# Kernel optimization log

Measured on AMD Instinct MI355X. Metric: run time of the kernel, lower is better.

## Reference

```python
import jax, jax.numpy as jnp
import numpy as np

B, S, D, H = 2, 2048, 1024, 16
HD = D // H  # head dim = 64

def setup_inputs() -> dict:
    key = jax.random.key(0)
    ks = jax.random.split(key, 3)
    scale = 1.0 / np.sqrt(D)
    return {
        "x": jax.random.normal(ks[0], (B, S, D), jnp.float32),
        "W_attn": jax.random.normal(ks[1], (D, 3 * D), jnp.float32) * scale,
        "b_attn": jnp.zeros((3 * D,), jnp.float32),
        "W_proj": jax.random.normal(ks[2], (D, D), jnp.float32) * scale,
        "b_proj": jnp.zeros((D,), jnp.float32),
    }

def reference(x, W_attn, b_attn, W_proj, b_proj):
    b, s, d = x.shape
    qkv = x @ W_attn + b_attn                      # [B,S,3D]
    q, k, v = jnp.split(qkv, 3, axis=-1)
    # [B,S,D] -> [B,H,S,HD]
    def heads(t):
        return t.reshape(b, s, H, HD).transpose(0, 2, 1, 3)
    q, k, v = heads(q), heads(k), heads(v)
    scores = jnp.einsum('bhqd,bhkd->bhqk', q, k) * (1.0 / np.sqrt(HD))
    causal = jnp.tril(jnp.ones((s, s), dtype=bool))
    scores = jnp.where(causal[None, None], scores, -jnp.inf)
    probs = jax.nn.softmax(scores, axis=-1)
    y = jnp.einsum('bhqk,bhkd->bhqd', probs, v)    # [B,H,S,HD]
    y = y.transpose(0, 2, 1, 3).reshape(b, s, d)
    return y @ W_proj + b_proj
```

## Files before the change

kernel.cpp:

```cpp
#include <hip/hip_runtime.h>

typedef __bf16 bf16;
typedef __bf16 bf16x4 __attribute__((ext_vector_type(4)));
typedef __bf16 bf16x8 __attribute__((ext_vector_type(8)));
typedef float f32x4 __attribute__((ext_vector_type(4)));

#define S_LEN 2048
#define D_DIM 1024
#define N_HEAD 16
#define HEAD_DIM 64
#define M_TOK 4096
#define BH 32

#define EXP2F(x) __builtin_amdgcn_exp2f(x)
#define Q_SCALE 0.18033688f

typedef __attribute__((address_space(3))) void lds_void;
typedef const __attribute__((address_space(1))) void gbl_void;

__device__ __forceinline__ void gl_lds16(const bf16* g, bf16* l) {
  __builtin_amdgcn_global_load_lds((gbl_void*)g, (lds_void*)l, 16, 0, 0);
}

__global__ __launch_bounds__(256) void k_cast(const float* __restrict__ x,
                                              bf16* __restrict__ o, int n) {
  int i = (blockIdx.x * 256 + threadIdx.x) * 4;
  if (i >= n) return;
  float4 v = *(const float4*)(x + i);
  bf16x4 w;
  w[0] = (bf16)v.x; w[1] = (bf16)v.y; w[2] = (bf16)v.z; w[3] = (bf16)v.w;
  *(bf16x4*)(o + i) = w;
}

__global__ __launch_bounds__(256) void k_transpose(const float* __restrict__ W,
                                                   bf16* __restrict__ Wt,
                                                   int K, int N) {
  __shared__ float tile[32][33];
  int nb = blockIdx.x, kb = blockIdx.y;
  int t = threadIdx.x;
  int r = t >> 3, c4 = (t & 7) * 4;
  float4 v = *(const float4*)&W[(kb * 32 + r) * N + nb * 32 + c4];
  tile[r][c4 + 0] = v.x; tile[r][c4 + 1] = v.y;
  tile[r][c4 + 2] = v.z; tile[r][c4 + 3] = v.w;
  __syncthreads();
  bf16x4 o;
  #pragma unroll
  for (int i = 0; i < 4; i++) o[i] = (bf16)tile[c4 + i][r];
  *(bf16x4*)&Wt[(nb * 32 + r) * K + kb * 32 + c4] = o;
}

__global__ __launch_bounds__(256, 2)
void k_gemm_qkv(const bf16* __restrict__ A, const bf16* __restrict__ Bt,
                const float* __restrict__ bias,
                bf16* __restrict__ qk, bf16* __restrict__ vT) {
  __shared__ bf16 As[128 * 32];
  __shared__ bf16 Bs[128 * 32];
  const int K = 1024;
  int bn = blockIdx.x, bm = blockIdx.y;
  int t = threadIdx.x;
  int wave = t >> 6, lane = t & 63, c = lane & 15, quad = lane >> 4;
  int wm = wave & 1, wn = wave >> 1;
  int ldrow = lane >> 2, ldcol = (lane & 3) * 8;

  const bf16* Ag = A + (size_t)(bm * 128) * K;
  const bf16* Bg = Bt + (size_t)(bn * 128) * K;

  f32x4 acc[4][4] = {};

  for (int k0 = 0; k0 < K; k0 += 32) {
    __syncthreads();
    #pragma unroll
    for (int q = 0; q < 2; q++) {
      int r0 = (wave * 2 + q) * 16;
      gl_lds16(&Ag[(size_t)(r0 + ldrow) * K + k0 + ldcol], &As[r0 * 32]);
      gl_lds16(&Bg[(size_t)(r0 + ldrow) * K + k0 + ldcol], &Bs[r0 * 32]);
    }
    __syncthreads();
    bf16x8 af[4];
    #pragma unroll
    for (int mt = 0; mt < 4; mt++)
      af[mt] = *(const bf16x8*)&As[(wm * 64 + mt * 16 + c) * 32 + quad * 8];
    #pragma unroll
    for (int nt = 0; nt < 4; nt++) {
      bf16x8 bfr = *(const bf16x8*)&Bs[(wn * 64 + nt * 16 + c) * 32 + quad * 8];
      #pragma unroll
      for (int mt = 0; mt < 4; mt++)
        acc[mt][nt] = __builtin_amdgcn_mfma_f32_16x16x32_bf16(af[mt], bfr, acc[mt][nt], 0, 0, 0);
    }
  }

  #pragma unroll
  for (int nt = 0; nt < 4; nt++) {
    int n = bn * 128 + wn * 64 + nt * 16 + c;
    int which = n >> 10, nl = n & 1023;
    int h = nl >> 6, hd = nl & 63;
    float bv = bias[n];
    #pragma unroll
    for (int mt = 0; mt < 4; mt++) {
      int m0 = bm * 128 + wm * 64 + mt * 16 + quad * 4;
      int b = m0 >> 11, s0 = m0 & 2047;
      int bh = b * N_HEAD + h;
      if (which == 2) {
        bf16x4 o;
        #pragma unroll
        for (int r = 0; r < 4; r++) o[r] = (bf16)(acc[mt][nt][r] + bv);
        *(bf16x4*)&vT[((size_t)bh * HEAD_DIM + hd) * S_LEN + s0] = o;
      } else if (which == 0) {
        #pragma unroll
        for (int r = 0; r < 4; r++)
          qk[(bh * S_LEN + s0 + r) * HEAD_DIM + hd] = (bf16)((acc[mt][nt][r] + bv) * Q_SCALE);
      } else {
        #pragma unroll
        for (int r = 0; r < 4; r++)
          qk[BH * S_LEN * HEAD_DIM + (bh * S_LEN + s0 + r) * HEAD_DIM + hd] = (bf16)(acc[mt][nt][r] + bv);
      }
    }
  }
}

__global__ __launch_bounds__(256, 2)
void k_attn(const bf16* __restrict__ qk, const bf16* __restrict__ vT,
            bf16* __restrict__ y) {
  __shared__ bf16 Ks[64][72];
  __shared__ bf16 Vs[64][72];
  __shared__ bf16 Ps[128][72];
  int bx = blockIdx.x;
  int bh = bx & 31;
  int tile = 15 - (bx >> 5);
  int t = threadIdx.x, w = t >> 6, lane = t & 63, c = lane & 15, quad = lane >> 4;
  const bf16* Qg = qk + (size_t)bh * (S_LEN * HEAD_DIM);
  const bf16* Kg = qk + (size_t)(BH + bh) * (S_LEN * HEAD_DIM);
  const bf16* Vg = vT + (size_t)bh * (HEAD_DIM * S_LEN);
  int b = bh >> 4, h = bh & 15;
  int srow = t >> 3, scol = (t & 7) * 8;

  int qA = tile * 128 + w * 16;
  int qB = qA + 64;
  int nkb = 2 * tile + 2;
  int dthr = w * 16 + c;

  bf16x8 qfA0 = *(const bf16x8*)&Qg[(qA + c) * HEAD_DIM + quad * 8];
  bf16x8 qfA1 = *(const bf16x8*)&Qg[(qA + c) * HEAD_DIM + 32 + quad * 8];
  bf16x8 qfB0 = *(const bf16x8*)&Qg[(qB + c) * HEAD_DIM + quad * 8];
  bf16x8 qfB1 = *(const bf16x8*)&Qg[(qB + c) * HEAD_DIM + 32 + quad * 8];

  float mA = -1e30f, lA = 0.f, mB = -1e30f, lB = 0.f;
  f32x4 accA[4] = {}, accB[4] = {};

  bf16x8 kr0 = *(const bf16x8*)&Kg[srow * HEAD_DIM + scol];
  bf16x8 kr1 = *(const bf16x8*)&Kg[(srow + 32) * HEAD_DIM + scol];
  bf16x8 vr0 = *(const bf16x8*)&Vg[(size_t)srow * S_LEN + scol];
  bf16x8 vr1 = *(const bf16x8*)&Vg[(size_t)(srow + 32) * S_LEN + scol];

  for (int kb = 0; kb < nkb; kb++) {
    __syncthreads();
    *(bf16x8*)&Ks[srow][scol] = kr0;
    *(bf16x8*)&Ks[srow + 32][scol] = kr1;
    *(bf16x8*)&Vs[srow][scol] = vr0;
    *(bf16x8*)&Vs[srow + 32][scol] = vr1;
    __syncthreads();
    if (kb + 1 < nkb) {
      kr0 = *(const bf16x8*)&Kg[((kb + 1) * 64 + srow) * HEAD_DIM + scol];
      kr1 = *(const bf16x8*)&Kg[((kb + 1) * 64 + srow + 32) * HEAD_DIM + scol];
      vr0 = *(const bf16x8*)&Vg[(size_t)srow * S_LEN + (kb + 1) * 64 + scol];
      vr1 = *(const bf16x8*)&Vg[(size_t)(srow + 32) * S_LEN + (kb + 1) * 64 + scol];
    }

    bool lastA = (kb == 2 * tile + 1);
    bool diagA = (kb == 2 * tile);
    bool diagB = (kb == 2 * tile + 1);

    f32x4 scA[4], scB[4];
    #pragma unroll
    for (int kt = 0; kt < 4; kt++) {
      bf16x8 kf0 = *(const bf16x8*)&Ks[kt * 16 + c][quad * 8];
      bf16x8 kf1 = *(const bf16x8*)&Ks[kt * 16 + c][32 + quad * 8];
      if (!lastA) {
        f32x4 z = {};
        z = __builtin_amdgcn_mfma_f32_16x16x32_bf16(kf0, qfA0, z, 0, 0, 0);
        z = __builtin_amdgcn_mfma_f32_16x16x32_bf16(kf1, qfA1, z, 0, 0, 0);
        scA[kt] = z;
      }
      f32x4 z = {};
      z = __builtin_amdgcn_mfma_f32_16x16x32_bf16(kf0, qfB0, z, 0, 0, 0);
      z = __builtin_amdgcn_mfma_f32_16x16x32_bf16(kf1, qfB1, z, 0, 0, 0);
      scB[kt] = z;
    }

    if (diagA) {
      #pragma unroll
      for (int kt = 0; kt < 4; kt++)
        #pragma unroll
        for (int r = 0; r < 4; r++)
          if (kt * 16 + quad * 4 + r > dthr) scA[kt][r] = -1e30f;
    }
    if (diagB) {
      #pragma unroll
      for (int kt = 0; kt < 4; kt++)
        #pragma unroll
        for (int r = 0; r < 4; r++)
          if (kt * 16 + quad * 4 + r > dthr) scB[kt][r] = -1e30f;
    }

    if (!lastA) {
      float mx = scA[0][0];
      #pragma unroll
      for (int kt = 0; kt < 4; kt++)
        #pragma unroll
        for (int r = 0; r < 4; r++) mx = fmaxf(mx, scA[kt][r]);
      mx = fmaxf(mx, __shfl_xor(mx, 16));
      mx = fmaxf(mx, __shfl_xor(mx, 32));
      float mnew = fmaxf(mA, mx);
      float alpha = EXP2F(mA - mnew);
      float sum = 0.f;
      #pragma unroll
      for (int kt = 0; kt < 4; kt++) {
        bf16x4 pk;
        #pragma unroll
        for (int r = 0; r < 4; r++) {
          float pv = EXP2F(scA[kt][r] - mnew);
          sum += pv;
          pk[r] = (bf16)pv;
        }
        *(bf16x4*)&Ps[w * 16 + c][kt * 16 + quad * 4] = pk;
      }
      sum += __shfl_xor(sum, 16);
      sum += __shfl_xor(sum, 32);
      lA = lA * alpha + sum;
      mA = mnew;
      #pragma unroll
      for (int dt = 0; dt < 4; dt++)
        #pragma unroll
        for (int r = 0; r < 4; r++) accA[dt][r] *= alpha;
    }

    {
      float mx = scB[0][0];
      #pragma unroll
      for (int kt = 0; kt < 4; kt++)
        #pragma unroll
        for (int r = 0; r < 4; r++) mx = fmaxf(mx, scB[kt][r]);
      mx = fmaxf(mx, __shfl_xor(mx, 16));
      mx = fmaxf(mx, __shfl_xor(mx, 32));
      float mnew = fmaxf(mB, mx);
      float alpha = EXP2F(mB - mnew);
      float sum = 0.f;
      #pragma unroll
      for (int kt = 0; kt < 4; kt++) {
        bf16x4 pk;
        #pragma unroll
        for (int r = 0; r < 4; r++) {
          float pv = EXP2F(scB[kt][r] - mnew);
          sum += pv;
          pk[r] = (bf16)pv;
        }
        *(bf16x4*)&Ps[64 + w * 16 + c][kt * 16 + quad * 4] = pk;
      }
      sum += __shfl_xor(sum, 16);
      sum += __shfl_xor(sum, 32);
      lB = lB * alpha + sum;
      mB = mnew;
      #pragma unroll
      for (int dt = 0; dt < 4; dt++)
        #pragma unroll
        for (int r = 0; r < 4; r++) accB[dt][r] *= alpha;
    }

    #pragma unroll
    for (int ks = 0; ks < 2; ks++) {
      bf16x8 pfB = *(const bf16x8*)&Ps[64 + w * 16 + c][ks * 32 + quad * 8];
      bf16x8 pfA;
      if (!lastA) pfA = *(const bf16x8*)&Ps[w * 16 + c][ks * 32 + quad * 8];
      #pragma unroll
      for (int dt = 0; dt < 4; dt++) {
        bf16x8 vf = *(const bf16x8*)&Vs[dt * 16 + c][ks * 32 + quad * 8];
        if (!lastA)
          accA[dt] = __builtin_amdgcn_mfma_f32_16x16x32_bf16(vf, pfA, accA[dt], 0, 0, 0);
        accB[dt] = __builtin_amdgcn_mfma_f32_16x16x32_bf16(vf, pfB, accB[dt], 0, 0, 0);
      }
    }
  }

  float liA = 1.0f / lA, liB = 1.0f / lB;
  #pragma unroll
  for (int dt = 0; dt < 4; dt++) {
    bf16x4 oA, oB;
    #pragma unroll
    for (int r = 0; r < 4; r++) {
      oA[r] = (bf16)(accA[dt][r] * liA);
      oB[r] = (bf16)(accB[dt][r] * liB);
    }
    *(bf16x4*)&y[((size_t)(b * S_LEN + qA + c) * N_HEAD + h) * HEAD_DIM + dt * 16 + quad * 4] = oA;
    *(bf16x4*)&y[((size_t)(b * S_LEN + qB + c) * N_HEAD + h) * HEAD_DIM + dt * 16 + quad * 4] = oB;
  }
}

__global__ __launch_bounds__(256, 2)
void k_gemm_proj(const bf16* __restrict__ A, const bf16* __restrict__ Bt,
                 const float* __restrict__ bias, float* __restrict__ out) {
  __shared__ bf16 As[128 * 32];
  __shared__ bf16 Bs[64 * 32];
  const int K = 1024;
  int bn = blockIdx.x, bm = blockIdx.y;
  int t = threadIdx.x;
  int wave = t >> 6, lane = t & 63, c = lane & 15, quad = lane >> 4;
  int wm = wave & 1, wn = wave >> 1;
  int ldrow = lane >> 2, ldcol = (lane & 3) * 8;

  const bf16* Ag = A + (size_t)(bm * 128) * K;
  const bf16* Bg = Bt + (size_t)(bn * 64) * K;

  f32x4 acc[4][2] = {};

  for (int k0 = 0; k0 < K; k0 += 32) {
    __syncthreads();
    #pragma unroll
    for (int q = 0; q < 2; q++) {
      int r0 = (wave * 2 + q) * 16;
      gl_lds16(&Ag[(size_t)(r0 + ldrow) * K + k0 + ldcol], &As[r0 * 32]);
    }
    gl_lds16(&Bg[(size_t)(wave * 16 + ldrow) * K + k0 + ldcol], &Bs[wave * 16 * 32]);
    __syncthreads();
    bf16x8 af[4];
    #pragma unroll
    for (int mt = 0; mt < 4; mt++)
      af[mt] = *(const bf16x8*)&As[(wm * 64 + mt * 16 + c) * 32 + quad * 8];
    #pragma unroll
    for (int nt = 0; nt < 2; nt++) {
      bf16x8 bfr = *(const bf16x8*)&Bs[(wn * 32 + nt * 16 + c) * 32 + quad * 8];
      #pragma unroll
      for (int mt = 0; mt < 4; mt++)
        acc[mt][nt] = __builtin_amdgcn_mfma_f32_16x16x32_bf16(af[mt], bfr, acc[mt][nt], 0, 0, 0);
    }
  }

  #pragma unroll
  for (int nt = 0; nt < 2; nt++) {
    int n = bn * 64 + wn * 32 + nt * 16 + c;
    float bv = bias[n];
    #pragma unroll
    for (int mt = 0; mt < 4; mt++) {
      #pragma unroll
      for (int r = 0; r < 4; r++) {
        int m = bm * 128 + wm * 64 + mt * 16 + quad * 4 + r;
        out[(size_t)m * D_DIM + n] = acc[mt][nt][r] + bv;
      }
    }
  }
}

extern "C" void kernel_launch(void* const* d_in, const int* in_sizes, int n_in,
                              void* d_out, int out_size, void* d_ws, size_t ws_size,
                              hipStream_t stream) {
  const float* x      = (const float*)d_in[0];
  const float* W_attn = (const float*)d_in[1];
  const float* b_attn = (const float*)d_in[2];
  const float* W_proj = (const float*)d_in[3];
  const float* b_proj = (const float*)d_in[4];
  float* out = (float*)d_out;

  bf16* x_bf = (bf16*)d_ws;
  bf16* wat  = x_bf + 4096 * 1024;
  bf16* wpt  = wat + 3072 * 1024;
  bf16* qk   = wpt + 1024 * 1024;
  bf16* vT   = qk + 8 * 1024 * 1024;
  bf16* y_bf = vT + 4 * 1024 * 1024;

  k_cast<<<4096, 256, 0, stream>>>(x, x_bf, 4096 * 1024);
  k_transpose<<<dim3(3072 / 32, 1024 / 32), 256, 0, stream>>>(W_attn, wat, 1024, 3072);
  k_transpose<<<dim3(1024 / 32, 1024 / 32), 256, 0, stream>>>(W_proj, wpt, 1024, 1024);
  k_gemm_qkv<<<dim3(24, 32), 256, 0, stream>>>(x_bf, wat, b_attn, qk, vT);
  k_attn<<<512, 256, 0, stream>>>(qk, vT, y_bf);
  k_gemm_proj<<<dim3(16, 32), 256, 0, stream>>>(y_bf, wpt, b_proj, out);
}
```

Baseline: 201.3 us.

## Balance causal attention work by pairing Q tiles and double-buffer K/V in swizzled LDS

Each attention block now handles two 64-row query tiles, p and 31-p, instead of one contiguous 128-row tile. Every block therefore does the same number of key blocks, which evens out causal load imbalance. K and V are double-buffered in LDS so one barrier per iteration suffices, with the next tile stored after compute. The padded LDS rows are replaced by an XOR swizzle to avoid bank conflicts while using less shared memory.

```diff
diff --git a/kernel.cpp b/kernel.cpp
--- a/kernel.cpp
+++ b/kernel.cpp
@@ -14,6 +14,8 @@
 
 #define EXP2F(x) __builtin_amdgcn_exp2f(x)
 #define Q_SCALE 0.18033688f
+
+#define SW(r, c) ((c) ^ (((r) & 3) << 4))
 
 typedef __attribute__((address_space(3))) void lds_void;
 typedef const __attribute__((address_space(1))) void gbl_void;
@@ -121,177 +123,167 @@
 __global__ __launch_bounds__(256, 2)
 void k_attn(const bf16* __restrict__ qk, const bf16* __restrict__ vT,
             bf16* __restrict__ y) {
-  __shared__ bf16 Ks[64][72];
-  __shared__ bf16 Vs[64][72];
-  __shared__ bf16 Ps[128][72];
+  __shared__ bf16 Ks[2][64][64];
+  __shared__ bf16 Vs[2][64][64];
+  __shared__ bf16 Ps[128][64];
   int bx = blockIdx.x;
   int bh = bx & 31;
-  int tile = 15 - (bx >> 5);
+  int p = bx >> 5;
   int t = threadIdx.x, w = t >> 6, lane = t & 63, c = lane & 15, quad = lane >> 4;
   const bf16* Qg = qk + (size_t)bh * (S_LEN * HEAD_DIM);
   const bf16* Kg = qk + (size_t)(BH + bh) * (S_LEN * HEAD_DIM);
   const bf16* Vg = vT + (size_t)bh * (HEAD_DIM * S_LEN);
   int b = bh >> 4, h = bh & 15;
   int srow = t >> 3, scol = (t & 7) * 8;
-
-  int qA = tile * 128 + w * 16;
-  int qB = qA + 64;
-  int nkb = 2 * tile + 2;
-  int dthr = w * 16 + c;
-
-  bf16x8 qfA0 = *(const bf16x8*)&Qg[(qA + c) * HEAD_DIM + quad * 8];
-  bf16x8 qfA1 = *(const bf16x8*)&Qg[(qA + c) * HEAD_DIM + 32 + quad * 8];
-  bf16x8 qfB0 = *(const bf16x8*)&Qg[(qB + c) * HEAD_DIM + quad * 8];
-  bf16x8 qfB1 = *(const bf16x8*)&Qg[(qB + c) * HEAD_DIM + 32 + quad * 8];
-
-  float mA = -1e30f, lA = 0.f, mB = -1e30f, lB = 0.f;
-  f32x4 accA[4] = {}, accB[4] = {};
+  int swcol = SW(srow, scol);
+
+  const int tileQ0 = p, tileQ1 = 31 - p;
+  const int nkb = 32 - p;
+  const int dthr = w * 16 + c;
+
+  bf16x8 qf[2][2];
+  f32x4 acc[2][4] = {};
+  float mM[2] = {-1e30f, -1e30f}, lL[2] = {0.f, 0.f};
+  {
+    int qr0 = tileQ0 * 64 + w * 16 + c;
+    int qr1 = tileQ1 * 64 + w * 16 + c;
+    qf[0][0] = *(const bf16x8*)&Qg[qr0 * HEAD_DIM + quad * 8];
+    qf[0][1] = *(const bf16x8*)&Qg[qr0 * HEAD_DIM + 32 + quad * 8];
+    qf[1][0] = *(const bf16x8*)&Qg[qr1 * HEAD_DIM + quad * 8];
+    qf[1][1] = *(const bf16x8*)&Qg[qr1 * HEAD_DIM + 32 + quad * 8];
+  }
 
   bf16x8 kr0 = *(const bf16x8*)&Kg[srow * HEAD_DIM + scol];
   bf16x8 kr1 = *(const bf16x8*)&Kg[(srow + 32) * HEAD_DIM + scol];
   bf16x8 vr0 = *(const bf16x8*)&Vg[(size_t)srow * S_LEN + scol];
   bf16x8 vr1 = *(const bf16x8*)&Vg[(size_t)(srow + 32) * S_LEN + scol];
+  *(bf16x8*)&Ks[0][srow][swcol] = kr0;
+  *(bf16x8*)&Ks[0][srow + 32][swcol] = kr1;
+  *(bf16x8*)&Vs[0][srow][swcol] = vr0;
+  *(bf16x8*)&Vs[0][srow + 32][swcol] = vr1;
 
   for (int kb = 0; kb < nkb; kb++) {
     __syncthreads();
-    *(bf16x8*)&Ks[srow][scol] = kr0;
-    *(bf16x8*)&Ks[srow + 32][scol] = kr1;
-    *(bf16x8*)&Vs[srow][scol] = vr0;
-    *(bf16x8*)&Vs[srow + 32][scol] = vr1;
-    __syncthreads();
-    if (kb + 1 < nkb) {
+    int cur = kb & 1;
+    bool haveNext = (kb + 1 < nkb);
+    if (haveNext) {
       kr0 = *(const bf16x8*)&Kg[((kb + 1) * 64 + srow) * HEAD_DIM + scol];
       kr1 = *(const bf16x8*)&Kg[((kb + 1) * 64 + srow + 32) * HEAD_DIM + scol];
       vr0 = *(const bf16x8*)&Vg[(size_t)srow * S_LEN + (kb + 1) * 64 + scol];
       vr1 = *(const bf16x8*)&Vg[(size_t)(srow + 32) * S_LEN + (kb + 1) * 64 + scol];
     }
 
-    bool lastA = (kb == 2 * tile + 1);
-    bool diagA = (kb == 2 * tile);
-    bool diagB = (kb == 2 * tile + 1);
-
-    f32x4 scA[4], scB[4];
+    bool act0 = (kb <= p);
+    bool dia0 = (kb == p);
+    bool dia1 = (kb == 31 - p);
+
+    f32x4 sc[2][4];
     #pragma unroll
     for (int kt = 0; kt < 4; kt++) {
-      bf16x8 kf0 = *(const bf16x8*)&Ks[kt * 16 + c][quad * 8];
-      bf16x8 kf1 = *(const bf16x8*)&Ks[kt * 16 + c][32 + quad * 8];
-      if (!lastA) {
+      int kr = kt * 16 + c;
+      bf16x8 kf0 = *(const bf16x8*)&Ks[cur][kr][SW(kr, quad * 8)];
+      bf16x8 kf1 = *(const bf16x8*)&Ks[cur][kr][SW(kr, 32 + quad * 8)];
+      if (act0) {
         f32x4 z = {};
-        z = __builtin_amdgcn_mfma_f32_16x16x32_bf16(kf0, qfA0, z, 0, 0, 0);
-        z = __builtin_amdgcn_mfma_f32_16x16x32_bf16(kf1, qfA1, z, 0, 0, 0);
-        scA[kt] = z;
+        z = __builtin_amdgcn_mfma_f32_16x16x32_bf16(kf0, qf[0][0], z, 0, 0, 0);
+        z = __builtin_amdgcn_mfma_f32_16x16x32_bf16(kf1, qf[0][1], z, 0, 0, 0);
+        sc[0][kt] = z;
       }
       f32x4 z = {};
-      z = __builtin_amdgcn_mfma_f32_16x16x32_bf16(kf0, qfB0, z, 0, 0, 0);
-      z = __builtin_amdgcn_mfma_f32_16x16x32_bf16(kf1, qfB1, z, 0, 0, 0);
-      scB[kt] = z;
-    }
-
-    if (diagA) {
+      z = __builtin_amdgcn_mfma_f32_16x16x32_bf16(kf0, qf[1][0], z, 0, 0, 0);
+      z = __builtin_amdgcn_mfma_f32_16x16x32_bf16(kf1, qf[1][1], z, 0, 0, 0);
+      sc[1][kt] = z;
+    }
+
+    if (dia0) {
       #pragma unroll
       for (int kt = 0; kt < 4; kt++)
         #pragma unroll
         for (int r = 0; r < 4; r++)
-          if (kt * 16 + quad * 4 + r > dthr) scA[kt][r] = -1e30f;
-    }
-    if (diagB) {
+          if (kt * 16 + quad * 4 + r > dthr) sc[0][kt][r] = -1e30f;
+    }
+    if (dia1) {
       #pragma unroll
       for (int kt = 0; kt < 4; kt++)
         #pragma unroll
         for (int r = 0; r < 4; r++)
-          if (kt * 16 + quad * 4 + r > dthr) scB[kt][r] = -1e30f;
-    }
-
-    if (!lastA) {
-      float mx = scA[0][0];
+          if (kt * 16 + quad * 4 + r > dthr) sc[1][kt][r] = -1e30f;
+    }
+
+    #pragma unroll
+    for (int st = 0; st < 2; st++) {
+      if (st == 0 && !act0) continue;
+      float mx = sc[st][0][0];
       #pragma unroll
       for (int kt = 0; kt < 4; kt++)
         #pragma unroll
-        for (int r = 0; r < 4; r++) mx = fmaxf(mx, scA[kt][r]);
+        for (int r = 0; r < 4; r++) mx = fmaxf(mx, sc[st][kt][r]);
       mx = fmaxf(mx, __shfl_xor(mx, 16));
       mx = fmaxf(mx, __shfl_xor(mx, 32));
-      float mnew = fmaxf(mA, mx);
-      float alpha = EXP2F(mA - mnew);
+      float mnew = fmaxf(mM[st], mx);
+      float alpha = EXP2F(mM[st] - mnew);
       float sum = 0.f;
+      int prow = st * 64 + w * 16 + c;
       #pragma unroll
       for (int kt = 0; kt < 4; kt++) {
         bf16x4 pk;
         #pragma unroll
         for (int r = 0; r < 4; r++) {
-          float pv = EXP2F(scA[kt][r] - mnew);
+          float pv = EXP2F(sc[st][kt][r] - mnew);
           sum += pv;
           pk[r] = (bf16)pv;
         }
-        *(bf16x4*)&Ps[w * 16 + c][kt * 16 + quad * 4] = pk;
+        *(bf16x4*)&Ps[prow][SW(prow, kt * 16 + quad * 4)] = pk;
       }
       sum += __shfl_xor(sum, 16);
       sum += __shfl_xor(sum, 32);
-      lA = lA * alpha + sum;
-      mA = mnew;
+      lL[st] = lL[st] * alpha + sum;
+      mM[st] = mnew;
       #pragma unroll
       for (int dt = 0; dt < 4; dt++)
         #pragma unroll
-        for (int r = 0; r < 4; r++) accA[dt][r] *= alpha;
-    }
-
-    {
-      float mx = scB[0][0];
-      #pragma unroll
-      for (int kt = 0; kt < 4; kt++)
-        #pragma unroll
-        for (int r = 0; r < 4; r++) mx = fmaxf(mx, scB[kt][r]);
-      mx = fmaxf(mx, __shfl_xor(mx, 16));
-      mx = fmaxf(mx, __shfl_xor(mx, 32));
-      float mnew = fmaxf(mB, mx);
-      float alpha = EXP2F(mB - mnew);
-      float sum = 0.f;
-      #pragma unroll
-      for (int kt = 0; kt < 4; kt++) {
-        bf16x4 pk;
-        #pragma unroll
-        for (int r = 0; r < 4; r++) {
-          float pv = EXP2F(scB[kt][r] - mnew);
-          sum += pv;
-          pk[r] = (bf16)pv;
-        }
-        *(bf16x4*)&Ps[64 + w * 16 + c][kt * 16 + quad * 4] = pk;
-      }
-      sum += __shfl_xor(sum, 16);
-      sum += __shfl_xor(sum, 32);
-      lB = lB * alpha + sum;
-      mB = mnew;
-      #pragma unroll
-      for (int dt = 0; dt < 4; dt++)
-        #pragma unroll
-        for (int r = 0; r < 4; r++) accB[dt][r] *= alpha;
+        for (int r = 0; r < 4; r++) acc[st][dt][r] *= alpha;
     }
 
     #pragma unroll
     for (int ks = 0; ks < 2; ks++) {
-      bf16x8 pfB = *(const bf16x8*)&Ps[64 + w * 16 + c][ks * 32 + quad * 8];
-      bf16x8 pfA;
-      if (!lastA) pfA = *(const bf16x8*)&Ps[w * 16 + c][ks * 32 + quad * 8];
+      int prow1 = 64 + w * 16 + c;
+      bf16x8 pf1 = *(const bf16x8*)&Ps[prow1][SW(prow1, ks * 32 + quad * 8)];
+      bf16x8 pf0;
+      if (act0) {
+        int prow0 = w * 16 + c;
+        pf0 = *(const bf16x8*)&Ps[prow0][SW(prow0, ks * 32 + quad * 8)];
+      }
       #pragma unroll
       for (int dt = 0; dt < 4; dt++) {
-        bf16x8 vf = *(const bf16x8*)&Vs[dt * 16 + c][ks * 32 + quad * 8];
-        if (!lastA)
-          accA[dt] = __builtin_amdgcn_mfma_f32_16x16x32_bf16(vf, pfA, accA[dt], 0, 0, 0);
-        accB[dt] = __builtin_amdgcn_mfma_f32_16x16x32_bf16(vf, pfB, accB[dt], 0, 0, 0);
-      }
-    }
-  }
-
-  float liA = 1.0f / lA, liB = 1.0f / lB;
+        int vrow = dt * 16 + c;
+        bf16x8 vf = *(const bf16x8*)&Vs[cur][vrow][SW(vrow, ks * 32 + quad * 8)];
+        if (act0)
+          acc[0][dt] = __builtin_amdgcn_mfma_f32_16x16x32_bf16(vf, pf0, acc[0][dt], 0, 0, 0);
+        acc[1][dt] = __builtin_amdgcn_mfma_f32_16x16x32_bf16(vf, pf1, acc[1][dt], 0, 0, 0);
+      }
+    }
+
+    if (haveNext) {
+      int nxt = cur ^ 1;
+      *(bf16x8*)&Ks[nxt][srow][swcol] = kr0;
+      *(bf16x8*)&Ks[nxt][srow + 32][swcol] = kr1;
+      *(bf16x8*)&Vs[nxt][srow][swcol] = vr0;
+      *(bf16x8*)&Vs[nxt][srow + 32][swcol] = vr1;
+    }
+  }
+
   #pragma unroll
-  for (int dt = 0; dt < 4; dt++) {
-    bf16x4 oA, oB;
-    #pragma unroll
-    for (int r = 0; r < 4; r++) {
-      oA[r] = (bf16)(accA[dt][r] * liA);
-      oB[r] = (bf16)(accB[dt][r] * liB);
-    }
-    *(bf16x4*)&y[((size_t)(b * S_LEN + qA + c) * N_HEAD + h) * HEAD_DIM + dt * 16 + quad * 4] = oA;
-    *(bf16x4*)&y[((size_t)(b * S_LEN + qB + c) * N_HEAD + h) * HEAD_DIM + dt * 16 + quad * 4] = oB;
+  for (int st = 0; st < 2; st++) {
+    int q = (st == 0 ? tileQ0 : tileQ1) * 64 + w * 16 + c;
+    float linv = 1.0f / lL[st];
+    #pragma unroll
+    for (int dt = 0; dt < 4; dt++) {
+      bf16x4 o;
+      #pragma unroll
+      for (int r = 0; r < 4; r++) o[r] = (bf16)(acc[st][dt][r] * linv);
+      *(bf16x4*)&y[((size_t)(b * S_LEN + q) * N_HEAD + h) * HEAD_DIM + dt * 16 + quad * 4] = o;
+    }
   }
 }
 
```

After: 189.4 us. 5.9% less time.
